# Optimization experiments

Measured on AMD Instinct MI355X. Metric: run time of the kernel, lower is better.

The kernel has to match this reference:

```python
import jax, jax.numpy as jnp
import numpy as np


def setup_inputs() -> dict:
    key = jax.random.key(0)
    k1, k2, k3 = jax.random.split(key, 3)
    B, N, D = 16, 2048, 128
    q = jax.random.normal(k1, (B, N, D), dtype=jnp.float32)
    k = jax.random.normal(k2, (B, D, N), dtype=jnp.float32)
    v = jax.random.normal(k3, (B, N, D), dtype=jnp.float32)
    return {"q": q, "k": k, "v": v}


def reference(q, k, v):
    # scores: [B, N, N] — note NO 1/sqrt(d) scaling, matching the source
    scores = jnp.einsum('bnd,bdm->bnm', q, k)
    probs = jax.nn.softmax(scores, axis=-1)
    out = jnp.einsum('bnm,bmd->bnd', probs, v)  # [B, N, D]
    return out
```

## Files before the change

kernel.cpp:

```cpp
#include <hip/hip_runtime.h>
#include <hip/hip_bf16.h>


typedef __attribute__((ext_vector_type(8))) _Float16 f16x8;
typedef __attribute__((ext_vector_type(16))) float f32x16;

constexpr int Bz = 16;
constexpr int Nn = 2048;
constexpr int Dd = 128;
constexpr int BM = 128;
constexpr int BN = 32;
constexpr int PK = 40;

__device__ __forceinline__ int swz(int r) { return (r ^ (r >> 3)) & 7; }
__device__ __forceinline__ int sw4(int d) { return ((d >> 1) ^ (d >> 3)) & 3; }

__device__ __forceinline__ uint packh2(float a, float b) {
    union { _Float16 h[2]; uint u; } p;
    p.h[0] = (_Float16)a; p.h[1] = (_Float16)b;
    return p.u;
}

__global__ __launch_bounds__(512, 2)
void fattn_kernel(const float* __restrict__ qg,
                  const float* __restrict__ kg,
                  const float* __restrict__ vg,
                  float* __restrict__ og)
{
    __shared__ ushort lds_k[2][BN * Dd];
    __shared__ ushort lds_v[2][Dd * BN];
    __shared__ ushort lds_p[4][32 * PK];

    const int bid  = blockIdx.x;
    const int xcd  = bid & 7;
    const int idx  = bid >> 3;
    const int b    = xcd * 2 + (idx >> 4);
    const int q0   = (idx & 15) * BM;
    const int tid  = threadIdx.x;
    const int wv   = tid >> 6;
    const int lane = tid & 63;
    const int h    = lane >> 5;
    const int l31  = lane & 31;
    const bool producer = (wv >= 4);

    const int ptid = (wv - 4) * 64 + lane;
    const int kgrp = ptid & 3;
    const int krow = ptid >> 2;
    const int vgrp = ptid & 15;
    const int vrow = ptid >> 4;
    const float* kbase = kg + (size_t)b * Dd * Nn;
    const float* vbase = vg + (size_t)b * Nn * Dd;
    float4 kr[4], vr[4];

    auto issue_loads = [&](int n0) {
        const int d0 = krow * 2;
        const float* s0 = kbase + (size_t)d0 * Nn + n0 + kgrp * 8;
        kr[0] = ((const float4*)s0)[0];
        kr[1] = ((const float4*)s0)[1];
        kr[2] = ((const float4*)(s0 + Nn))[0];
        kr[3] = ((const float4*)(s0 + Nn))[1];
        const int kk0 = vrow * 2;
        const float* t0 = vbase + (size_t)(n0 + kk0) * Dd + vgrp * 8;
        vr[0] = ((const float4*)t0)[0];
        vr[1] = ((const float4*)t0)[1];
        vr[2] = ((const float4*)(t0 + Dd))[0];
        vr[3] = ((const float4*)(t0 + Dd))[1];
    };
    auto write_lds = [&](int buf) {
        uint* kw = (uint*)lds_k[buf];
        const float* av = (const float*)&kr[0];
        const float* bv = (const float*)&kr[2];
        #pragma unroll
        for (int j = 0; j < 8; ++j) {
            const int n = kgrp * 8 + j;
            kw[n * (Dd / 2) + (krow ^ (swz(n) << 2))] = packh2(av[j], bv[j]);
        }
        uint* vw = (uint*)lds_v[buf];
        const float* cv = (const float*)&vr[0];
        const float* dv = (const float*)&vr[2];
        #pragma unroll
        for (int j = 0; j < 8; ++j) {
            const int dd = vgrp * 8 + j;
            vw[dd * (BN / 2) + (vrow ^ (sw4(dd) << 2))] = packh2(cv[j], dv[j]);
        }
    };

    f16x8 qf[8];
    if (!producer) {
        const float* qp = qg + (size_t)(b * Nn + q0 + wv * 32 + l31) * Dd + h * 8;
        #pragma unroll
        for (int c = 0; c < 8; ++c) {
            float4 x0 = *(const float4*)(qp + c * 16);
            float4 x1 = *(const float4*)(qp + c * 16 + 4);
            const float xv[8] = {x0.x, x0.y, x0.z, x0.w, x1.x, x1.y, x1.z, x1.w};
            union { f16x8 v; _Float16 e[8]; } u;
            #pragma unroll
            for (int j = 0; j < 8; ++j) u.e[j] = (_Float16)xv[j];
            qf[c] = u.v;
        }
    }
    f32x16 accO[4];
    #pragma unroll
    for (int dt = 0; dt < 4; ++dt)
        #pragma unroll
        for (int r = 0; r < 16; ++r) accO[dt][r] = 0.f;
    float m_i = -1e30f, l_i = 0.f;

    if (producer) {
        issue_loads(0);
        write_lds(0);
    }
    __syncthreads();

    constexpr int ITERS = Nn / BN;
    for (int it = 0; it < ITERS; ++it) {
        const int cur = it & 1;
        if (producer) {
            if (it + 1 < ITERS) {
                issue_loads((it + 1) * BN);
                write_lds(cur ^ 1);
            }
        } else {
            const ushort* kb = lds_k[cur];
            const ushort* vb = lds_v[cur];

            f32x16 accS;
            #pragma unroll
            for (int r = 0; r < 16; ++r) accS[r] = 0.f;
            {
                const int kkrow = l31;
                const int sw = swz(kkrow) << 3;
                #pragma unroll
                for (int c = 0; c < 8; ++c) {
                    f16x8 kf = *(const f16x8*)&kb[kkrow * Dd + ((c * 16 + h * 8) ^ sw)];
                    accS = __builtin_amdgcn_mfma_f32_32x32x16_f16(kf, qf[c], accS, 0, 0, 0);
                }
            }

            float mx = accS[0];
            #pragma unroll
            for (int r = 1; r < 16; ++r) mx = fmaxf(mx, accS[r]);
            mx = fmaxf(mx, __shfl_xor(mx, 32, 64));
            const float mn = fmaxf(m_i, mx);
            const float alpha = __expf(m_i - mn);
            m_i = mn;
            float local = 0.f;
            #pragma unroll
            for (int r = 0; r < 16; ++r) {
                const float p = __expf(accS[r] - mn);
                accS[r] = p;
                local += p;
            }
            l_i = l_i * alpha + local;
            #pragma unroll
            for (int dt = 0; dt < 4; ++dt)
                #pragma unroll
                for (int r = 0; r < 16; ++r) accO[dt][r] *= alpha;

            ushort* pl = lds_p[wv];
            #pragma unroll
            for (int g = 0; g < 4; ++g) {
                uint2 w;
                w.x = packh2(accS[4 * g + 0], accS[4 * g + 1]);
                w.y = packh2(accS[4 * g + 2], accS[4 * g + 3]);
                *(uint2*)(pl + l31 * PK + 8 * g + 4 * h) = w;
            }
            f16x8 pf0 = *(const f16x8*)&pl[l31 * PK + 8 * h];
            f16x8 pf1 = *(const f16x8*)&pl[l31 * PK + 16 + 8 * h];

            #pragma unroll
            for (int dt = 0; dt < 4; ++dt) {
                const int drow = dt * 32 + l31;
                const int sv = sw4(drow) << 3;
                f16x8 vf0 = *(const f16x8*)&vb[drow * BN + ((8 * h) ^ sv)];
                f16x8 vf1 = *(const f16x8*)&vb[drow * BN + ((16 + 8 * h) ^ sv)];
                accO[dt] = __builtin_amdgcn_mfma_f32_32x32x16_f16(vf0, pf0, accO[dt], 0, 0, 0);
                accO[dt] = __builtin_amdgcn_mfma_f32_32x32x16_f16(vf1, pf1, accO[dt], 0, 0, 0);
            }
        }
        __syncthreads();
    }

    if (!producer) {
        float l = l_i + __shfl_xor(l_i, 32, 64);
        const float inv = 1.f / l;
        float* ob = og + (size_t)(b * Nn + q0 + wv * 32 + l31) * Dd;
        #pragma unroll
        for (int dt = 0; dt < 4; ++dt) {
            #pragma unroll
            for (int g = 0; g < 4; ++g) {
                float4 val;
                val.x = accO[dt][4 * g + 0] * inv;
                val.y = accO[dt][4 * g + 1] * inv;
                val.z = accO[dt][4 * g + 2] * inv;
                val.w = accO[dt][4 * g + 3] * inv;
                *(float4*)(ob + dt * 32 + 8 * g + 4 * h) = val;
            }
        }
    }
}

extern "C" void kernel_launch(void* const* d_in, const int* in_sizes, int n_in,
                              void* d_out, int out_size, void* d_ws, size_t ws_size,
                              hipStream_t stream) {
    const float* q = (const float*)d_in[0];
    const float* k = (const float*)d_in[1];
    const float* v = (const float*)d_in[2];
    float* o = (float*)d_out;
    (void)d_ws; (void)ws_size; (void)in_sizes; (void)n_in; (void)out_size;
    fattn_kernel<<<dim3(Bz * (Nn / BM)), dim3(512), 0, stream>>>(q, k, v, o);
}
```

Measured before the change: 145.0 us.

## Halve query tile to 64 rows with 2 consumer and 2 producer waves

Shrinks each block to 64 query rows, served by 2 consumer waves and 2 producer waves (256 threads), and doubles the grid to 512 blocks. Each producer thread now loads and converts two passes of the K/V tile, and launch bounds target 4 blocks per CU. The aim is more blocks in flight and better occupancy balance across CUs. The cost is that every K/V tile is fetched and converted twice as often per query row, raising global traffic and producer work relative to MFMA work.

After: 395.1 us. 2.72x slower.

```diff
diff --git a/kernel.cpp b/kernel.cpp
--- a/kernel.cpp
+++ b/kernel.cpp
@@ -8,7 +8,7 @@
 constexpr int Bz = 16;
 constexpr int Nn = 2048;
 constexpr int Dd = 128;
-constexpr int BM = 128;
+constexpr int BM = 64;
 constexpr int BN = 32;
 constexpr int PK = 40;
 
@@ -21,7 +21,7 @@
     return p.u;
 }
 
-__global__ __launch_bounds__(512, 2)
+__global__ __launch_bounds__(256, 4)
 void fattn_kernel(const float* __restrict__ qg,
                   const float* __restrict__ kg,
                   const float* __restrict__ vg,
@@ -29,59 +29,67 @@
 {
     __shared__ ushort lds_k[2][BN * Dd];
     __shared__ ushort lds_v[2][Dd * BN];
-    __shared__ ushort lds_p[4][32 * PK];
+    __shared__ ushort lds_p[2][32 * PK];
 
     const int bid  = blockIdx.x;
     const int xcd  = bid & 7;
     const int idx  = bid >> 3;
-    const int b    = xcd * 2 + (idx >> 4);
-    const int q0   = (idx & 15) * BM;
+    const int b    = xcd * 2 + (idx >> 5);
+    const int q0   = (idx & 31) * BM;
     const int tid  = threadIdx.x;
     const int wv   = tid >> 6;
     const int lane = tid & 63;
     const int h    = lane >> 5;
     const int l31  = lane & 31;
-    const bool producer = (wv >= 4);
-
-    const int ptid = (wv - 4) * 64 + lane;
+    const bool producer = (wv >= 2);
+
+    const int ptid = (wv - 2) * 64 + lane;
     const int kgrp = ptid & 3;
     const int krow = ptid >> 2;
     const int vgrp = ptid & 15;
     const int vrow = ptid >> 4;
     const float* kbase = kg + (size_t)b * Dd * Nn;
     const float* vbase = vg + (size_t)b * Nn * Dd;
-    float4 kr[4], vr[4];
+    float4 kr[8], vr[8];
 
     auto issue_loads = [&](int n0) {
-        const int d0 = krow * 2;
-        const float* s0 = kbase + (size_t)d0 * Nn + n0 + kgrp * 8;
-        kr[0] = ((const float4*)s0)[0];
-        kr[1] = ((const float4*)s0)[1];
-        kr[2] = ((const float4*)(s0 + Nn))[0];
-        kr[3] = ((const float4*)(s0 + Nn))[1];
-        const int kk0 = vrow * 2;
-        const float* t0 = vbase + (size_t)(n0 + kk0) * Dd + vgrp * 8;
-        vr[0] = ((const float4*)t0)[0];
-        vr[1] = ((const float4*)t0)[1];
-        vr[2] = ((const float4*)(t0 + Dd))[0];
-        vr[3] = ((const float4*)(t0 + Dd))[1];
+        #pragma unroll
+        for (int pass = 0; pass < 2; ++pass) {
+            const int d0 = (krow + pass * 32) * 2;
+            const float* s0 = kbase + (size_t)d0 * Nn + n0 + kgrp * 8;
+            kr[pass * 4 + 0] = ((const float4*)s0)[0];
+            kr[pass * 4 + 1] = ((const float4*)s0)[1];
+            kr[pass * 4 + 2] = ((const float4*)(s0 + Nn))[0];
+            kr[pass * 4 + 3] = ((const float4*)(s0 + Nn))[1];
+            const int kk0 = (vrow + pass * 8) * 2;
+            const float* t0 = vbase + (size_t)(n0 + kk0) * Dd + vgrp * 8;
+            vr[pass * 4 + 0] = ((const float4*)t0)[0];
+            vr[pass * 4 + 1] = ((const float4*)t0)[1];
+            vr[pass * 4 + 2] = ((const float4*)(t0 + Dd))[0];
+            vr[pass * 4 + 3] = ((const float4*)(t0 + Dd))[1];
+        }
     };
     auto write_lds = [&](int buf) {
         uint* kw = (uint*)lds_k[buf];
-        const float* av = (const float*)&kr[0];
-        const float* bv = (const float*)&kr[2];
-        #pragma unroll
-        for (int j = 0; j < 8; ++j) {
-            const int n = kgrp * 8 + j;
-            kw[n * (Dd / 2) + (krow ^ (swz(n) << 2))] = packh2(av[j], bv[j]);
-        }
         uint* vw = (uint*)lds_v[buf];
-        const float* cv = (const float*)&vr[0];
-        const float* dv = (const float*)&vr[2];
-        #pragma unroll
-        for (int j = 0; j < 8; ++j) {
-            const int dd = vgrp * 8 + j;
-            vw[dd * (BN / 2) + (vrow ^ (sw4(dd) << 2))] = packh2(cv[j], dv[j]);
+        #pragma unroll
+        for (int pass = 0; pass < 2; ++pass) {
+            const int dp = krow + pass * 32;
+            const float* av = (const float*)&kr[pass * 4 + 0];
+            const float* bv = (const float*)&kr[pass * 4 + 2];
+            #pragma unroll
+            for (int j = 0; j < 8; ++j) {
+                const int n = kgrp * 8 + j;
+                kw[n * (Dd / 2) + (dp ^ (swz(n) << 2))] = packh2(av[j], bv[j]);
+            }
+            const int kp = vrow + pass * 8;
+            const float* cv = (const float*)&vr[pass * 4 + 0];
+            const float* dv = (const float*)&vr[pass * 4 + 2];
+            #pragma unroll
+            for (int j = 0; j < 8; ++j) {
+                const int dd = vgrp * 8 + j;
+                vw[dd * (BN / 2) + (kp ^ (sw4(dd) << 2))] = packh2(cv[j], dv[j]);
+            }
         }
     };
 
@@ -208,5 +216,5 @@
     const float* v = (const float*)d_in[2];
     float* o = (float*)d_out;
     (void)d_ws; (void)ws_size; (void)in_sizes; (void)n_in; (void)out_size;
-    fattn_kernel<<<dim3(Bz * (Nn / BM)), dim3(512), 0, stream>>>(q, k, v, o);
+    fattn_kernel<<<dim3(Bz * (Nn / BM)), dim3(256), 0, stream>>>(q, k, v, o);
 }
```
